# Kernel optimization log

Hardware: AMD Instinct MI355X
Metric: run time of the kernel (lower is better)

## Reference

```python
import jax, jax.numpy as jnp
import numpy as np

R, B, F, H, C = 32, 2048, 512, 1024, 100  # n_rules, batch, n_fea, 2*n_fea, n_cls


def setup_inputs() -> dict:
    key = jax.random.key(0)
    ks = jax.random.split(key, 10)
    sc = lambda k, shape, fan: (jax.random.normal(k, shape, jnp.float32) / np.float32(np.sqrt(fan)))
    return {
        "data": jax.random.normal(ks[0], (B, F), jnp.float32),
        "proto": jax.random.normal(ks[1], (R, F), jnp.float32),
        "var": jax.random.uniform(ks[2], (R, F), jnp.float32, 0.5, 1.5),
        "fs_w1": sc(ks[3], (F, H), F), "fs_b1": jnp.zeros((H,), jnp.float32),
        "fs_w2": sc(ks[4], (H, F), H), "fs_b2": jnp.zeros((F,), jnp.float32),
        "fs_w3": sc(ks[5], (F, 1), F), "fs_b3": jnp.zeros((1,), jnp.float32),
        "cq_w1": sc(ks[6], (R, F, H), F), "cq_b1": jnp.zeros((R, H), jnp.float32),
        "cq_w2": sc(ks[7], (R, H, F), H), "cq_b2": jnp.zeros((R, F), jnp.float32),
        "cq_w3": sc(ks[8], (R, F, C), F), "cq_b3": jnp.zeros((R, C), jnp.float32),
        "is_train": 1,
    }


def reference(data, proto, var, fs_w1, fs_b1, fs_w2, fs_b2, fs_w3, fs_b3,
              cq_w1, cq_b1, cq_w2, cq_b2, cq_w3, cq_b3, is_train):
    # Gaussian fuzzy membership per rule: [R, B, F]
    fuzzy = jnp.exp(-(data[None, :, :] - proto[:, None, :]) ** 2
                    / (2.0 * var[:, None, :] ** 2))
    # shared fire-strength MLP applied per rule
    h = jax.nn.relu(jnp.einsum('rbf,fh->rbh', fuzzy, fs_w1) + fs_b1)
    h = jax.nn.relu(jnp.einsum('rbh,hf->rbf', h, fs_w2) + fs_b2)
    fs_logits = (jnp.einsum('rbf,fo->rbo', h, fs_w3) + fs_b3)[..., 0]  # [R, B]
    fire = jax.nn.softmax(fs_logits.T, axis=1)  # [B, R], softmax over rules
    # per-rule consequent MLPs on raw data (grouped GEMMs)
    g = jax.nn.relu(jnp.einsum('bf,rfh->rbh', data, cq_w1) + cq_b1[:, None, :])
    g = jax.nn.relu(jnp.einsum('rbh,rhf->rbf', g, cq_w2) + cq_b2[:, None, :])
    logits = jnp.einsum('rbf,rfc->rbc', g, cq_w3) + cq_b3[:, None, :]  # [R, B, C]
    # softmax-weighted expert sum, then class softmax
    out = jnp.einsum('br,rbc->bc', fire, logits)  # [B, C]
    return jax.nn.softmax(out, axis=1)
```

## Files before the change

### kernel.cpp

```cpp
#include <hip/hip_runtime.h>

typedef __attribute__((ext_vector_type(8))) short short8;
typedef __attribute__((ext_vector_type(4))) float f32x4;

__device__ __forceinline__ unsigned short f2bf(float f) {
    union { float f; unsigned u; } v; v.f = f;
    unsigned r = v.u + 0x7FFFu + ((v.u >> 16) & 1u);
    return (unsigned short)(r >> 16);
}

__global__ __launch_bounds__(256)
void transpose_kernel(const float* __restrict__ X, unsigned short* __restrict__ Y,
                      int K, int N, int Np) {
    __shared__ float tile[32][33];
    int g = blockIdx.z;
    const float* Xg = X + (long)g * K * N;
    unsigned short* Yg = Y + (long)g * Np * K;
    int k0 = blockIdx.x * 32, n0 = blockIdx.y * 32;
    int tx = threadIdx.x & 31, ty = threadIdx.x >> 5;
#pragma unroll
    for (int i = 0; i < 4; ++i) {
        int kk = ty + i * 8;
        int n = n0 + tx;
        tile[kk][tx] = (n < N) ? Xg[(long)(k0 + kk) * N + n] : 0.0f;
    }
    __syncthreads();
#pragma unroll
    for (int i = 0; i < 4; ++i) {
        int nn = ty + i * 8;
        Yg[(long)(n0 + nn) * K + k0 + tx] = f2bf(tile[tx][nn]);
    }
}

__global__ __launch_bounds__(256)
void fuzzy_kernel(const float* __restrict__ data, const float* __restrict__ proto,
                  const float* __restrict__ var, unsigned short* __restrict__ fuzzy,
                  unsigned short* __restrict__ data_bf) {
    int t = threadIdx.x;
    int rb = blockIdx.x * 2 + (t >> 7);
    int r = rb >> 11, b = rb & 2047;
    int f = (t & 127) * 4;
    float4 d = *(const float4*)(data + (long)b * 512 + f);
    float4 p = *(const float4*)(proto + (long)r * 512 + f);
    float4 w = *(const float4*)(var + (long)r * 512 + f);
    ushort4 o;
    float x;
    x = d.x - p.x; o.x = f2bf(__expf(-(x * x) / (2.f * w.x * w.x)));
    x = d.y - p.y; o.y = f2bf(__expf(-(x * x) / (2.f * w.y * w.y)));
    x = d.z - p.z; o.z = f2bf(__expf(-(x * x) / (2.f * w.z * w.z)));
    x = d.w - p.w; o.w = f2bf(__expf(-(x * x) / (2.f * w.w * w.w)));
    *(ushort4*)(fuzzy + (long)rb * 512 + f) = o;
    if (r == 0) {
        ushort4 od;
        od.x = f2bf(d.x); od.y = f2bf(d.y); od.z = f2bf(d.z); od.w = f2bf(d.w);
        *(ushort4*)(data_bf + (long)b * 512 + f) = od;
    }
}

#define RING_WAIT_BARRIER(n)                                        \
    asm volatile("s_waitcnt vmcnt(" #n ")" ::: "memory");           \
    __builtin_amdgcn_sched_barrier(0);                              \
    __builtin_amdgcn_s_barrier();                                   \
    __builtin_amdgcn_sched_barrier(0);

template<int EPI, bool RELU>
__global__ __launch_bounds__(512, 2)
void gemm256_kernel(const unsigned short* __restrict__ A,
                    const unsigned short* __restrict__ Bt,
                    const float* __restrict__ bias,
                    void* __restrict__ Cptr,
                    const float* __restrict__ w3,
                    float* __restrict__ fslog,
                    int nM, int nN, int K,
                    long sAg, long sBg, long sCg, int sBiasG) {
    unsigned tot = gridDim.x, bid = blockIdx.x;
    unsigned sw = (bid & 7u) * (tot >> 3) + (bid >> 3);
    unsigned pg = (unsigned)(nM * nN);
    unsigned g = sw / pg;
    unsigned rem = sw - g * pg;
    const int m0 = (int)(rem / (unsigned)nN) * 256;
    const int n0 = (int)(rem % (unsigned)nN) * 256;
    const int N = nN * 256;
    A += (long)g * sAg; Bt += (long)g * sBg; bias += (long)g * sBiasG;

    __shared__ __align__(16) unsigned short lds[8][8192];

    const int tid = threadIdx.x;
    const int lane = tid & 63;
    const int w = tid >> 6;
    const int wm = w >> 2, wn = w & 3;
    const int r16 = lane & 15, kg = lane >> 4;

    f32x4 acc[8][4];
#pragma unroll
    for (int i = 0; i < 8; ++i)
#pragma unroll
        for (int j = 0; j < 4; ++j) {
            f32x4 z = {0.f, 0.f, 0.f, 0.f};
            acc[i][j] = z;
        }

    const int nsteps = K >> 5;

    auto STAGE = [&](int slot, int kt) {
        const int k0 = kt << 5;
#pragma unroll
        for (int j = 0; j < 2; ++j) {
            int f = j * 512 + tid;
            int row = f >> 2, sl = f & 3;
            int kk = (sl ^ ((row >> 1) & 3)) << 3;
            const unsigned short* ga = A + (long)(m0 + row) * K + k0 + kk;
            __builtin_amdgcn_global_load_lds(
                (const __attribute__((address_space(1))) void*)ga,
                (__attribute__((address_space(3))) void*)(&lds[slot][0] + (j * 512 + w * 64) * 8),
                16, 0, 0);
            const unsigned short* gb = Bt + (long)(n0 + row) * K + k0 + kk;
            __builtin_amdgcn_global_load_lds(
                (const __attribute__((address_space(1))) void*)gb,
                (__attribute__((address_space(3))) void*)(&lds[4 + slot][0] + (j * 512 + w * 64) * 8),
                16, 0, 0);
        }
    };

    auto COMPUTE = [&](int slot) {
        short8 aF[8], bF[4];
#pragma unroll
        for (int mt = 0; mt < 8; ++mt) {
            int R = wm * 128 + mt * 16 + r16;
            aF[mt] = *(const short8*)(&lds[slot][0] + R * 32 + ((kg ^ ((R >> 1) & 3)) << 3));
        }
#pragma unroll
        for (int nt = 0; nt < 4; ++nt) {
            int R = wn * 64 + nt * 16 + r16;
            bF[nt] = *(const short8*)(&lds[4 + slot][0] + R * 32 + ((kg ^ ((R >> 1) & 3)) << 3));
        }
        __builtin_amdgcn_s_setprio(1);
#pragma unroll
        for (int mt = 0; mt < 8; ++mt)
#pragma unroll
            for (int nt = 0; nt < 4; ++nt)
                acc[mt][nt] = __builtin_amdgcn_mfma_f32_16x16x32_bf16(
                    aF[mt], bF[nt], acc[mt][nt], 0, 0, 0);
        __builtin_amdgcn_s_setprio(0);
        asm volatile("" ::: "memory");
        __builtin_amdgcn_s_barrier();
        __builtin_amdgcn_sched_barrier(0);
    };

    STAGE(0, 0); STAGE(1, 1); STAGE(2, 2);
    for (int t = 0; t <= nsteps - 3; ++t) {
        if (t + 3 < nsteps) STAGE((t + 3) & 3, t + 3);
        RING_WAIT_BARRIER(8);
        COMPUTE(t & 3);
    }
    { RING_WAIT_BARRIER(4); COMPUTE((nsteps - 2) & 3); }
    { RING_WAIT_BARRIER(0); COMPUTE((nsteps - 1) & 3); }

    if constexpr (EPI == 1) {
        float w3v[4], bv[4];
#pragma unroll
        for (int nt = 0; nt < 4; ++nt) {
            int col = n0 + wn * 64 + nt * 16 + r16;
            w3v[nt] = w3[col];
            bv[nt] = bias[col];
        }
#pragma unroll
        for (int mt = 0; mt < 8; ++mt) {
#pragma unroll
            for (int j = 0; j < 4; ++j) {
                float p = 0.f;
#pragma unroll
                for (int nt = 0; nt < 4; ++nt) {
                    float v = acc[mt][nt][j] + bv[nt];
                    if (RELU) v = fmaxf(v, 0.f);
                    p += v * w3v[nt];
                }
                p += __shfl_xor(p, 1, 64);
                p += __shfl_xor(p, 2, 64);
                p += __shfl_xor(p, 4, 64);
                p += __shfl_xor(p, 8, 64);
                if (r16 == 0) {
                    int row = m0 + wm * 128 + mt * 16 + kg * 4 + j;
                    atomicAdd(&fslog[row], p);
                }
            }
        }
    } else {
        unsigned short* ldsC = &lds[0][0];
        float bv[4];
#pragma unroll
        for (int nt = 0; nt < 4; ++nt) bv[nt] = bias[n0 + wn * 64 + nt * 16 + r16];
#pragma unroll
        for (int mt = 0; mt < 8; ++mt) {
            int rr = wm * 128 + mt * 16 + kg * 4;
#pragma unroll
            for (int nt = 0; nt < 4; ++nt) {
                int cc = wn * 64 + nt * 16 + r16;
#pragma unroll
                for (int j = 0; j < 4; ++j) {
                    float v = acc[mt][nt][j] + bv[nt];
                    if (RELU) v = fmaxf(v, 0.f);
                    ldsC[(rr + j) * 256 + cc] = f2bf(v);
                }
            }
        }
        __syncthreads();
        unsigned short* Cg = (unsigned short*)Cptr + (long)g * sCg;
#pragma unroll
        for (int rnd = 0; rnd < 16; ++rnd) {
            int idx = rnd * 512 + tid;
            int row = idx >> 5;
            int c8 = idx & 31;
            short8 vv = *(const short8*)(ldsC + row * 256 + c8 * 8);
            *(short8*)(Cg + (long)(m0 + row) * N + n0 + c8 * 8) = vv;
        }
    }
}

template<int EPI, bool RELU>
__global__ __launch_bounds__(256, 2)
void gemm_kernel(const unsigned short* __restrict__ A,
                 const unsigned short* __restrict__ Bt,
                 const float* __restrict__ bias,
                 void* __restrict__ Cptr,
                 int nM, int nN, int K,
                 long sAg, long sBg, long sCg, int sBiasG, int biasN,
                 const float* __restrict__ fire, float* __restrict__ mix, int r0) {
    unsigned tot = gridDim.x;
    unsigned bid = blockIdx.x;
    unsigned sw = (tot & 7u) == 0 ? (bid & 7u) * (tot >> 3) + (bid >> 3) : bid;
    unsigned pg = (unsigned)nM * (unsigned)nN;
    unsigned g = sw / pg;
    unsigned rem = sw - g * pg;
    unsigned mt_ = rem / (unsigned)nN;
    unsigned nt_ = rem - mt_ * (unsigned)nN;
    const int N = nN * 128;
    A += (long)g * sAg;
    Bt += (long)g * sBg;
    bias += (long)g * sBiasG;
    const int m0 = (int)mt_ * 128;
    const int n0 = (int)nt_ * 128;

    __shared__ __align__(16) unsigned short ldsA[128 * 32];
    __shared__ __align__(16) unsigned short ldsB[128 * 32];

    const int tid = threadIdx.x;
    const int lane = tid & 63;
    const int w = tid >> 6;
    const int wm = w >> 1, wn = w & 1;
    const int r16 = lane & 15, kg = lane >> 4;

    f32x4 acc[4][4];
#pragma unroll
    for (int i = 0; i < 4; ++i)
#pragma unroll
        for (int j = 0; j < 4; ++j) {
            f32x4 z = {0.f, 0.f, 0.f, 0.f};
            acc[i][j] = z;
        }

    for (int k0 = 0; k0 < K; k0 += 32) {
#pragma unroll
        for (int j = 0; j < 2; ++j) {
            int t = j * 256 + tid;
            int row = t >> 2, kc = (t & 3) * 8;
            const unsigned short* ga = A + (long)(m0 + row) * K + k0 + kc;
            __builtin_amdgcn_global_load_lds(
                (const __attribute__((address_space(1))) void*)ga,
                (__attribute__((address_space(3))) void*)(ldsA + (j * 256 + w * 64) * 8),
                16, 0, 0);
            const unsigned short* gb = Bt + (long)(n0 + row) * K + k0 + kc;
            __builtin_amdgcn_global_load_lds(
                (const __attribute__((address_space(1))) void*)gb,
                (__attribute__((address_space(3))) void*)(ldsB + (j * 256 + w * 64) * 8),
                16, 0, 0);
        }
        __syncthreads();
        short8 aF[4], bF[4];
#pragma unroll
        for (int mt = 0; mt < 4; ++mt)
            aF[mt] = *(const short8*)(ldsA + (wm * 64 + mt * 16 + r16) * 32 + kg * 8);
#pragma unroll
        for (int nt = 0; nt < 4; ++nt)
            bF[nt] = *(const short8*)(ldsB + (wn * 64 + nt * 16 + r16) * 32 + kg * 8);
#pragma unroll
        for (int mt = 0; mt < 4; ++mt)
#pragma unroll
            for (int nt = 0; nt < 4; ++nt)
                acc[mt][nt] = __builtin_amdgcn_mfma_f32_16x16x32_bf16(
                    aF[mt], bF[nt], acc[mt][nt], 0, 0, 0);
        __syncthreads();
    }

    if constexpr (EPI == 3) {
        float bv[4];
#pragma unroll
        for (int nt = 0; nt < 4; ++nt) {
            int col = n0 + wn * 64 + nt * 16 + r16;
            bv[nt] = (col < biasN) ? bias[col] : 0.f;
        }
#pragma unroll
        for (int mt = 0; mt < 4; ++mt) {
#pragma unroll
            for (int j = 0; j < 4; ++j) {
                int row = m0 + wm * 64 + mt * 16 + kg * 4 + j;
                float f = fire[row * 32 + r0 + (int)g];
#pragma unroll
                for (int nt = 0; nt < 4; ++nt) {
                    int col = n0 + wn * 64 + nt * 16 + r16;
                    float v = acc[mt][nt][j] + bv[nt];
                    atomicAdd(&mix[row * 128 + col], f * v);
                }
            }
        }
    } else {
#pragma unroll
        for (int nt = 0; nt < 4; ++nt) {
            int col = n0 + wn * 64 + nt * 16 + r16;
            float bv = (col < biasN) ? bias[col] : 0.f;
#pragma unroll
            for (int mt = 0; mt < 4; ++mt) {
#pragma unroll
                for (int j = 0; j < 4; ++j) {
                    int row = m0 + wm * 64 + mt * 16 + kg * 4 + j;
                    float v = acc[mt][nt][j] + bv;
                    if (RELU) v = fmaxf(v, 0.f);
                    ((float*)Cptr)[(long)g * sCg + (long)row * N + col] = v;
                }
            }
        }
    }
}

__global__ __launch_bounds__(256)
void fire_kernel(const float* __restrict__ fslog, float* __restrict__ fire) {
    int b = blockIdx.x * 256 + threadIdx.x;
    float v[32];
    float mx = -1e30f;
#pragma unroll
    for (int r = 0; r < 32; ++r) { v[r] = fslog[r * 2048 + b]; mx = fmaxf(mx, v[r]); }
    float s = 0.f;
#pragma unroll
    for (int r = 0; r < 32; ++r) { v[r] = __expf(v[r] - mx); s += v[r]; }
    float inv = 1.f / s;
#pragma unroll
    for (int r = 0; r < 32; ++r) fire[b * 32 + r] = v[r] * inv;
}

__global__ __launch_bounds__(128)
void softmax_out_kernel(const float* __restrict__ mix, float* __restrict__ out) {
    int b = blockIdx.x, c = threadIdx.x;
    __shared__ float redm[2], reds[2];
    float val = (c < 100) ? mix[b * 128 + c] : -1e30f;
    float m = val;
#pragma unroll
    for (int off = 32; off; off >>= 1) m = fmaxf(m, __shfl_xor(m, off, 64));
    int lane = c & 63, wv = c >> 6;
    if (lane == 0) redm[wv] = m;
    __syncthreads();
    m = fmaxf(redm[0], redm[1]);
    float e = (c < 100) ? __expf(val - m) : 0.f;
    float s = e;
#pragma unroll
    for (int off = 32; off; off >>= 1) s += __shfl_xor(s, off, 64);
    if (lane == 0) reds[wv] = s;
    __syncthreads();
    s = reds[0] + reds[1];
    if (c < 100) out[b * 100 + c] = e / s;
}

extern "C" void kernel_launch(void* const* d_in, const int* in_sizes, int n_in,
                              void* d_out, int out_size, void* d_ws, size_t ws_size,
                              hipStream_t stream) {
    const float* data  = (const float*)d_in[0];
    const float* proto = (const float*)d_in[1];
    const float* var   = (const float*)d_in[2];
    const float* fs_w1 = (const float*)d_in[3];
    const float* fs_b1 = (const float*)d_in[4];
    const float* fs_w2 = (const float*)d_in[5];
    const float* fs_b2 = (const float*)d_in[6];
    const float* fs_w3 = (const float*)d_in[7];
    const float* cq_w1 = (const float*)d_in[9];
    const float* cq_b1 = (const float*)d_in[10];
    const float* cq_w2 = (const float*)d_in[11];
    const float* cq_b2 = (const float*)d_in[12];
    const float* cq_w3 = (const float*)d_in[13];
    const float* cq_b3 = (const float*)d_in[14];
    float* out = (float*)d_out;

    const size_t PERSIST = 2097152 + 1048576 + 1048576 + 262144 + 262144 + 1048576;
    const size_t H1SZ = (size_t)65536 * 1024 * 2;
    const size_t FUZZSZ = (size_t)65536 * 512 * 2;
    auto need = [&](int p) -> size_t {
        size_t fz = FUZZSZ > (size_t)p * 2097152 ? FUZZSZ : (size_t)p * 2097152;
        return PERSIST + H1SZ + fz + (size_t)p * (1048576 + 1048576 + 131072);
    };
    int p2r = 16;
    while (need(p2r) > ws_size && p2r > 2) p2r >>= 1;

    char* ws = (char*)d_ws;
    size_t off = 0;
    auto take = [&](size_t bytes) { char* p = ws + off; off += bytes; return p; };
    unsigned short* data_bf = (unsigned short*)take(2097152);
    unsigned short* w1t     = (unsigned short*)take(1048576);
    unsigned short* w2t     = (unsigned short*)take(1048576);
    float*          fslog   = (float*)take(262144);
    float*          fire    = (float*)take(262144);
    float*          mix     = (float*)take(1048576);
    unsigned short* h1      = (unsigned short*)take(H1SZ);
    size_t fzsz = FUZZSZ > (size_t)p2r * 2097152 ? FUZZSZ : (size_t)p2r * 2097152;
    unsigned short* fuzzy   = (unsigned short*)take(fzsz);
    unsigned short* cW1t    = (unsigned short*)take((size_t)p2r * 1048576);
    unsigned short* cW2t    = (unsigned short*)take((size_t)p2r * 1048576);
    unsigned short* cW3t    = (unsigned short*)take((size_t)p2r * 131072);
    unsigned short* g1 = h1;
    unsigned short* g2 = fuzzy;

    transpose_kernel<<<dim3(16, 32, 1), 256, 0, stream>>>(fs_w1, w1t, 512, 1024, 1024);
    transpose_kernel<<<dim3(32, 16, 1), 256, 0, stream>>>(fs_w2, w2t, 1024, 512, 512);
    hipMemsetAsync(fslog, 0, 262144, stream);
    hipMemsetAsync(mix, 0, 1048576, stream);

    fuzzy_kernel<<<32768, 256, 0, stream>>>(data, proto, var, fuzzy, data_bf);
    gemm256_kernel<0, true><<<256 * 4, 512, 0, stream>>>(
        fuzzy, w1t, fs_b1, h1, nullptr, nullptr, 256, 4, 512, 0, 0, 0, 0);
    gemm256_kernel<1, true><<<256 * 2, 512, 0, stream>>>(
        h1, w2t, fs_b2, nullptr, fs_w3, fslog, 256, 2, 1024, 0, 0, 0, 0);
    fire_kernel<<<8, 256, 0, stream>>>(fslog, fire);

    for (int ch = 0; ch < 32 / p2r; ++ch) {
        const int r0 = ch * p2r;
        transpose_kernel<<<dim3(16, 32, p2r), 256, 0, stream>>>(
            cq_w1 + (long)r0 * 512 * 1024, cW1t, 512, 1024, 1024);
        transpose_kernel<<<dim3(32, 16, p2r), 256, 0, stream>>>(
            cq_w2 + (long)r0 * 1024 * 512, cW2t, 1024, 512, 512);
        transpose_kernel<<<dim3(16, 4, p2r), 256, 0, stream>>>(
            cq_w3 + (long)r0 * 512 * 100, cW3t, 512, 100, 128);
        gemm256_kernel<0, true><<<8 * 4 * p2r, 512, 0, stream>>>(
            data_bf, cW1t, cq_b1 + (long)r0 * 1024, g1, nullptr, nullptr,
            8, 4, 512, 0, (long)1024 * 512, (long)2048 * 1024, 1024);
        gemm256_kernel<0, true><<<8 * 2 * p2r, 512, 0, stream>>>(
            g1, cW2t, cq_b2 + (long)r0 * 512, g2, nullptr, nullptr,
            8, 2, 1024, (long)2048 * 1024, (long)512 * 1024, (long)2048 * 512, 512);
        gemm_kernel<3, false><<<16 * 1 * p2r, 256, 0, stream>>>(
            g2, cW3t, cq_b3 + (long)r0 * 100, nullptr,
            16, 1, 512, (long)2048 * 512, (long)128 * 512, 0, 100, 100,
            fire, mix, r0);
    }
    softmax_out_kernel<<<2048, 128, 0, stream>>>(mix, out);
}
```

Measured before the change: 519.2 us.

## Store intermediate activations in 256x256 tiled layout for contiguous tile writes and reads

Intermediate GEMM outputs (h1, g1, g2) are now written as contiguous 256x256 blocks instead of row-major, so each block's epilogue store is one linear sweep. Downstream GEMMs read their A operand using the tiled addressing with row stride 256. This is meant to improve write coalescing and read locality between the chained GEMMs. Loads from a tile now span fewer DRAM pages, but the addressing is more complex and every producer/consumer pair must agree on the layout.

```diff
diff --git a/kernel.cpp b/kernel.cpp
--- a/kernel.cpp
+++ b/kernel.cpp
@@ -72,7 +72,8 @@
                     const float* __restrict__ w3,
                     float* __restrict__ fslog,
                     int nM, int nN, int K,
-                    long sAg, long sBg, long sCg, int sBiasG) {
+                    long sAg, long sBg, long sCg, int sBiasG,
+                    int aT, int cT) {
     unsigned tot = gridDim.x, bid = blockIdx.x;
     unsigned sw = (bid & 7u) * (tot >> 3) + (bid >> 3);
     unsigned pg = (unsigned)(nM * nN);
@@ -101,15 +102,19 @@
         }
 
     const int nsteps = K >> 5;
+    const long aRowStride = aT ? 256 : K;
 
     auto STAGE = [&](int slot, int kt) {
         const int k0 = kt << 5;
+        const long aBase = aT
+            ? (((long)((m0 >> 8) * (K >> 8) + (k0 >> 8))) << 16) + (k0 & 255)
+            : (long)m0 * K + k0;
 #pragma unroll
         for (int j = 0; j < 2; ++j) {
             int f = j * 512 + tid;
             int row = f >> 2, sl = f & 3;
             int kk = (sl ^ ((row >> 1) & 3)) << 3;
-            const unsigned short* ga = A + (long)(m0 + row) * K + k0 + kk;
+            const unsigned short* ga = A + aBase + (long)row * aRowStride + kk;
             __builtin_amdgcn_global_load_lds(
                 (const __attribute__((address_space(1))) void*)ga,
                 (__attribute__((address_space(3))) void*)(&lds[slot][0] + (j * 512 + w * 64) * 8),
@@ -206,13 +211,23 @@
         }
         __syncthreads();
         unsigned short* Cg = (unsigned short*)Cptr + (long)g * sCg;
-#pragma unroll
-        for (int rnd = 0; rnd < 16; ++rnd) {
-            int idx = rnd * 512 + tid;
-            int row = idx >> 5;
-            int c8 = idx & 31;
-            short8 vv = *(const short8*)(ldsC + row * 256 + c8 * 8);
-            *(short8*)(Cg + (long)(m0 + row) * N + n0 + c8 * 8) = vv;
+        if (cT) {
+            unsigned short* Ct = Cg + (((long)((m0 >> 8) * (N >> 8) + (n0 >> 8))) << 16);
+#pragma unroll
+            for (int rnd = 0; rnd < 16; ++rnd) {
+                int idx = rnd * 512 + tid;
+                short8 vv = *(const short8*)(ldsC + idx * 8);
+                *(short8*)(Ct + (long)idx * 8) = vv;
+            }
+        } else {
+#pragma unroll
+            for (int rnd = 0; rnd < 16; ++rnd) {
+                int idx = rnd * 512 + tid;
+                int row = idx >> 5;
+                int c8 = idx & 31;
+                short8 vv = *(const short8*)(ldsC + row * 256 + c8 * 8);
+                *(short8*)(Cg + (long)(m0 + row) * N + n0 + c8 * 8) = vv;
+            }
         }
     }
 }
@@ -225,7 +240,8 @@
                  void* __restrict__ Cptr,
                  int nM, int nN, int K,
                  long sAg, long sBg, long sCg, int sBiasG, int biasN,
-                 const float* __restrict__ fire, float* __restrict__ mix, int r0) {
+                 const float* __restrict__ fire, float* __restrict__ mix, int r0,
+                 int aT) {
     unsigned tot = gridDim.x;
     unsigned bid = blockIdx.x;
     unsigned sw = (tot & 7u) == 0 ? (bid & 7u) * (tot >> 3) + (bid >> 3) : bid;
@@ -259,12 +275,17 @@
             acc[i][j] = z;
         }
 
+    const long aRowStride = aT ? 256 : K;
+
     for (int k0 = 0; k0 < K; k0 += 32) {
+        const long aBase = aT
+            ? (((long)((m0 >> 8) * (K >> 8) + (k0 >> 8))) << 16) + (long)(m0 & 255) * 256 + (k0 & 255)
+            : (long)m0 * K + k0;
 #pragma unroll
         for (int j = 0; j < 2; ++j) {
             int t = j * 256 + tid;
             int row = t >> 2, kc = (t & 3) * 8;
-            const unsigned short* ga = A + (long)(m0 + row) * K + k0 + kc;
+            const unsigned short* ga = A + aBase + (long)row * aRowStride + kc;
             __builtin_amdgcn_global_load_lds(
                 (const __attribute__((address_space(1))) void*)ga,
                 (__attribute__((address_space(3))) void*)(ldsA + (j * 256 + w * 64) * 8),
@@ -423,9 +444,9 @@
 
     fuzzy_kernel<<<32768, 256, 0, stream>>>(data, proto, var, fuzzy, data_bf);
     gemm256_kernel<0, true><<<256 * 4, 512, 0, stream>>>(
-        fuzzy, w1t, fs_b1, h1, nullptr, nullptr, 256, 4, 512, 0, 0, 0, 0);
+        fuzzy, w1t, fs_b1, h1, nullptr, nullptr, 256, 4, 512, 0, 0, 0, 0, 0, 1);
     gemm256_kernel<1, true><<<256 * 2, 512, 0, stream>>>(
-        h1, w2t, fs_b2, nullptr, fs_w3, fslog, 256, 2, 1024, 0, 0, 0, 0);
+        h1, w2t, fs_b2, nullptr, fs_w3, fslog, 256, 2, 1024, 0, 0, 0, 0, 1, 0);
     fire_kernel<<<8, 256, 0, stream>>>(fslog, fire);
 
     for (int ch = 0; ch < 32 / p2r; ++ch) {
@@ -438,14 +459,14 @@
             cq_w3 + (long)r0 * 512 * 100, cW3t, 512, 100, 128);
         gemm256_kernel<0, true><<<8 * 4 * p2r, 512, 0, stream>>>(
             data_bf, cW1t, cq_b1 + (long)r0 * 1024, g1, nullptr, nullptr,
-            8, 4, 512, 0, (long)1024 * 512, (long)2048 * 1024, 1024);
+            8, 4, 512, 0, (long)1024 * 512, (long)2048 * 1024, 1024, 0, 1);
         gemm256_kernel<0, true><<<8 * 2 * p2r, 512, 0, stream>>>(
             g1, cW2t, cq_b2 + (long)r0 * 512, g2, nullptr, nullptr,
-            8, 2, 1024, (long)2048 * 1024, (long)512 * 1024, (long)2048 * 512, 512);
+            8, 2, 1024, (long)2048 * 1024, (long)512 * 1024, (long)2048 * 512, 512, 1, 1);
         gemm_kernel<3, false><<<16 * 1 * p2r, 256, 0, stream>>>(
             g2, cW3t, cq_b3 + (long)r0 * 100, nullptr,
             16, 1, 512, (long)2048 * 512, (long)128 * 512, 0, 100, 100,
-            fire, mix, r0);
+            fire, mix, r0, 1);
     }
     softmax_out_kernel<<<2048, 128, 0, stream>>>(mix, out);
 }
```

Measured after the change: 523.0 us. About the same (+0.7%).
